# Kernel tuning notes

Measured on AMD Instinct MI355X. Metric: run time of the kernel, lower is better.

The kernel has to match this reference:

```python
import jax, jax.numpy as jnp
import numpy as np


def setup_inputs() -> dict:
    key = jax.random.key(0)
    k1, k2 = jax.random.split(key)
    B, T, F = 16, 4096, 512
    x = jax.random.normal(k1, (B, T, F), dtype=jnp.float32)
    probs = jax.random.uniform(k2, (B,), dtype=jnp.float32)  # per-row CDF value
    return {"x": x, "probs": probs}


def reference(x, probs):
    # SMALL_VALUE_MASKING + SUM_BASED scaling (training=True path).
    B = x.shape[0]
    n = x[0].size  # elements per batch row (time*feat)
    flat = x.reshape(B, -1)
    sorted_flat = jnp.sort(flat, axis=1)
    # index = max(ceil(n * prob) - 1, 0), per batch row
    idx = jnp.maximum(jnp.ceil(jnp.float32(n) * probs).astype(jnp.int32) - 1, 0)
    threshold = jnp.take_along_axis(sorted_flat, idx[:, None], axis=1)  # [B,1]
    threshold = threshold.reshape((B,) + (1,) * (x.ndim - 1))  # [B,1,1]
    # mask = 1 - (x < threshold): zero out values strictly below the quantile
    mask = 1.0 - (x < threshold).astype(x.dtype)
    out = x * mask
    # sum-based rescaling: |sum(x) / sum(out)| per row, divide_no_nan semantics
    reduce_axes = tuple(range(1, x.ndim))
    num = jnp.sum(x, axis=reduce_axes)
    den = jnp.sum(out, axis=reduce_axes)
    scale = jnp.abs(jnp.where(den == 0, jnp.zeros_like(num), num / den))
    scale = scale.reshape((B,) + (1,) * (x.ndim - 1))
    return scale * out
```

## Files before the change

### kernel.cpp

```cpp
#include <hip/hip_runtime.h>
#include <stdint.h>

#define THREADS 256
#define EPB     65536
#define NBINS   4096
#define ITERS   (EPB / 4 / THREADS)
#define CNT_STRIDE 16
#define LDSCAP  8192
#define K4T     1024

typedef float vfloat4 __attribute__((ext_vector_type(4)));

__device__ __forceinline__ uint32_t f2u(float f) {
    uint32_t b = __float_as_uint(f);
    return (b & 0x80000000u) ? ~b : (b | 0x80000000u);
}
__device__ __forceinline__ float u2f(uint32_t u) {
    uint32_t b = (u & 0x80000000u) ? (u & 0x7FFFFFFFu) : ~u;
    return __uint_as_float(b);
}

__device__ __forceinline__ double blockReduceSum(double v) {
    for (int off = 32; off > 0; off >>= 1) v += __shfl_down(v, off, 64);
    __shared__ double wsum[16];
    int lane = threadIdx.x & 63, wid = threadIdx.x >> 6;
    if (lane == 0) wsum[wid] = v;
    __syncthreads();
    double r = 0.0;
    if (threadIdx.x == 0) {
        int nw = (int)(blockDim.x >> 6);
        for (int i = 0; i < nw; ++i) r += wsum[i];
    }
    return r;
}

__global__ void __launch_bounds__(THREADS) k0_zero(uint4* __restrict__ p, int n16) {
    int idx = blockIdx.x * THREADS + threadIdx.x;
    int stride = gridDim.x * THREADS;
    uint4 z = {0u, 0u, 0u, 0u};
    for (int i = idx; i < n16; i += stride) p[i] = z;
}

__global__ void __launch_bounds__(THREADS) k1_hist(
    const float* __restrict__ x, uint32_t* __restrict__ ghist,
    double* __restrict__ rowSum, int blocksPerRow, int n) {
    __shared__ uint32_t hist[NBINS];
    for (int i = threadIdx.x; i < NBINS; i += THREADS) hist[i] = 0;
    __syncthreads();

    int row   = blockIdx.x / blocksPerRow;
    int chunk = blockIdx.x % blocksPerRow;
    const float4* p = (const float4*)(x + (size_t)row * n + (size_t)chunk * EPB);

    double s = 0.0;
    #pragma unroll 4
    for (int it = 0; it < ITERS; ++it) {
        float4 v = p[it * THREADS + threadIdx.x];
        s += (double)v.x + (double)v.y + (double)v.z + (double)v.w;
        atomicAdd(&hist[f2u(v.x) >> 20], 1u);
        atomicAdd(&hist[f2u(v.y) >> 20], 1u);
        atomicAdd(&hist[f2u(v.z) >> 20], 1u);
        atomicAdd(&hist[f2u(v.w) >> 20], 1u);
    }
    __syncthreads();

    uint32_t* gh = ghist + (size_t)row * NBINS;
    for (int i = threadIdx.x; i < NBINS; i += THREADS) {
        uint32_t c = hist[i];
        if (c) atomicAdd(&gh[i], c);
    }
    double bs = blockReduceSum(s);
    if (threadIdx.x == 0) atomicAdd(&rowSum[row], bs);
}

__global__ void __launch_bounds__(THREADS) k2_select(
    const uint32_t* __restrict__ ghist, const float* __restrict__ probs,
    uint32_t* __restrict__ aStar, uint32_t* __restrict__ rankW, int n) {
    int row = blockIdx.x;
    const uint32_t* h = ghist + (size_t)row * NBINS;
    __shared__ uint32_t part[THREADS];
    uint32_t s = 0;
    #pragma unroll
    for (int i = 0; i < NBINS / THREADS; ++i) s += h[threadIdx.x * (NBINS / THREADS) + i];
    part[threadIdx.x] = s;
    __syncthreads();
    if (threadIdx.x == 0) {
        float p = probs[row];
        float t = ceilf((float)n * p);
        long long idx = (long long)t - 1;
        if (idx < 0) idx = 0;
        uint32_t k = (uint32_t)idx + 1;
        uint32_t cum = 0;
        int chunk = 0;
        for (; chunk < THREADS - 1; ++chunk) {
            if (cum + part[chunk] >= k) break;
            cum += part[chunk];
        }
        int bin = chunk * (NBINS / THREADS);
        for (;; ++bin) {
            uint32_t c = h[bin];
            if (cum + c >= k || bin == NBINS - 1) break;
            cum += c;
        }
        aStar[row] = (uint32_t)bin;
        rankW[row] = k - cum;
    }
}

__global__ void __launch_bounds__(THREADS) k3_cand(
    const float* __restrict__ x, const uint32_t* __restrict__ aStar,
    uint32_t* __restrict__ cand, uint32_t* __restrict__ candCount,
    double* __restrict__ rowSumGt, int blocksPerRow, int cap, int n) {
    __shared__ uint32_t lbuf[LDSCAP];
    __shared__ uint32_t lcnt;
    __shared__ uint32_t gbase;
    if (threadIdx.x == 0) lcnt = 0;
    __syncthreads();

    int row   = blockIdx.x / blocksPerRow;
    int chunk = blockIdx.x % blocksPerRow;
    uint32_t a = aStar[row];
    uint32_t* cl = cand + (size_t)row * cap;
    uint32_t* cc = candCount + (size_t)row * CNT_STRIDE;
    const float4* p = (const float4*)(x + (size_t)row * n + (size_t)chunk * EPB);

    double s = 0.0;
    #pragma unroll 4
    for (int it = 0; it < ITERS; ++it) {
        float4 v = p[it * THREADS + threadIdx.x];
        float vals[4] = {v.x, v.y, v.z, v.w};
        #pragma unroll
        for (int j = 0; j < 4; ++j) {
            uint32_t u = f2u(vals[j]);
            uint32_t b = u >> 20;
            if (b > a) s += (double)vals[j];
            else if (b == a) {
                uint32_t pos = atomicAdd(&lcnt, 1u);
                if (pos < LDSCAP) lbuf[pos] = u;
                else {
                    uint32_t g = atomicAdd(cc, 1u);
                    if ((int)g < cap) cl[g] = u;
                }
            }
        }
    }
    __syncthreads();
    uint32_t cnt = (lcnt < LDSCAP) ? lcnt : LDSCAP;
    if (threadIdx.x == 0) gbase = atomicAdd(cc, cnt);
    __syncthreads();
    uint32_t base = gbase;
    for (uint32_t i = threadIdx.x; i < cnt; i += THREADS) {
        uint32_t g = base + i;
        if ((int)g < cap) cl[g] = lbuf[i];
    }
    double bs = blockReduceSum(s);
    if (threadIdx.x == 0) atomicAdd(&rowSumGt[row], bs);
}

__global__ void __launch_bounds__(K4T) k4_final(
    const uint32_t* __restrict__ cand, const uint32_t* __restrict__ candCount,
    const uint32_t* __restrict__ aStar, const uint32_t* __restrict__ rankW,
    const double* __restrict__ rowSum, const double* __restrict__ rowSumGt,
    float* __restrict__ scaleArr, float* __restrict__ thrArr, int cap) {
    int row = blockIdx.x, tid = threadIdx.x;
    uint32_t c = candCount[(size_t)row * CNT_STRIDE];
    if (c > (uint32_t)cap) c = (uint32_t)cap;
    const uint32_t* cl = cand + (size_t)row * cap;

    __shared__ uint32_t hcnt[4096];
    __shared__ double   hsum[4096];
    __shared__ uint32_t part1[K4T];
    __shared__ uint32_t part2[64];
    __shared__ uint32_t cnt256[256];
    __shared__ double   sum256[256];
    __shared__ uint32_t sh_b1, sh_r2, sh_b2;

    for (int i = tid; i < 4096; i += K4T) { hcnt[i] = 0; hsum[i] = 0.0; }
    for (int i = tid; i < 256;  i += K4T) { cnt256[i] = 0; sum256[i] = 0.0; }
    __syncthreads();

    for (uint32_t i = tid; i < c; i += K4T) {
        uint32_t u = cl[i];
        uint32_t b = (u >> 8) & 0xFFFu;
        atomicAdd(&hcnt[b], 1u);
        atomicAdd(&hsum[b], (double)u2f(u));
    }
    __syncthreads();

    uint32_t p1 = hcnt[tid*4] + hcnt[tid*4+1] + hcnt[tid*4+2] + hcnt[tid*4+3];
    part1[tid] = p1;
    __syncthreads();
    if (tid < 64) {
        uint32_t s2 = 0;
        for (int j = 0; j < 16; ++j) s2 += part1[tid*16 + j];
        part2[tid] = s2;
    }
    __syncthreads();
    if (tid == 0) {
        uint32_t r = rankW[row];
        uint32_t cum = 0;
        int j = 0;
        for (; j < 63; ++j) { if (cum + part2[j] >= r) break; cum += part2[j]; }
        int t = j * 16;
        for (; t < j*16 + 15; ++t) { if (cum + part1[t] >= r) break; cum += part1[t]; }
        int b = t * 4;
        for (; b < t*4 + 3; ++b) { if (cum + hcnt[b] >= r) break; cum += hcnt[b]; }
        sh_b1 = (uint32_t)b;
        sh_r2 = r - cum;
    }
    __syncthreads();
    uint32_t b1 = sh_b1;

    double g = 0.0;
    for (int i = tid; i < 4096; i += K4T) if (i > (int)b1) g += hsum[i];

    for (uint32_t i = tid; i < c; i += K4T) {
        uint32_t u = cl[i];
        if (((u >> 8) & 0xFFFu) == b1) {
            atomicAdd(&cnt256[u & 0xFFu], 1u);
            atomicAdd(&sum256[u & 0xFFu], (double)u2f(u));
        }
    }
    __syncthreads();
    if (tid == 0) {
        uint32_t r2 = sh_r2, cum = 0;
        int b = 0;
        for (; b < 255; ++b) { if (cum + cnt256[b] >= r2) break; cum += cnt256[b]; }
        sh_b2 = (uint32_t)b;
    }
    __syncthreads();
    uint32_t b2 = sh_b2;
    uint32_t uthr = (aStar[row] << 20) | (b1 << 8) | b2;

    double g2 = 0.0;
    for (int i = tid; i < 256; i += K4T) if (i > (int)b2) g2 += sum256[i];

    double tot = blockReduceSum(g + g2);
    if (tid == 0) {
        tot += (double)cnt256[b2] * (double)u2f(uthr);
        double den = rowSumGt[row] + tot;
        double num = rowSum[row];
        double sc  = (den == 0.0) ? 0.0 : fabs(num / den);
        scaleArr[row] = (float)sc;
        thrArr[row]   = u2f(uthr);
    }
}

__global__ void __launch_bounds__(THREADS) k5_out(
    const float* __restrict__ x, float* __restrict__ out,
    const float* __restrict__ scaleArr, const float* __restrict__ thrArr,
    int blocksPerRow, int n) {
    int row   = blockIdx.x / blocksPerRow;
    int chunk = blockIdx.x % blocksPerRow;
    float sc = scaleArr[row];
    float th = thrArr[row];
    size_t base = (size_t)row * n + (size_t)chunk * EPB;
    const float4* p = (const float4*)(x + base);
    vfloat4* o = (vfloat4*)(out + base);
    #pragma unroll 4
    for (int it = 0; it < ITERS; ++it) {
        float4 v = p[it * THREADS + threadIdx.x];
        vfloat4 w;
        w.x = (v.x < th) ? 0.0f : v.x * sc;
        w.y = (v.y < th) ? 0.0f : v.y * sc;
        w.z = (v.z < th) ? 0.0f : v.z * sc;
        w.w = (v.w < th) ? 0.0f : v.w * sc;
        __builtin_nontemporal_store(w, &o[it * THREADS + threadIdx.x]);
    }
}

extern "C" void kernel_launch(void* const* d_in, const int* in_sizes, int n_in,
                              void* d_out, int out_size, void* d_ws, size_t ws_size,
                              hipStream_t stream) {
    const float* x     = (const float*)d_in[0];
    const float* probs = (const float*)d_in[1];
    float* out = (float*)d_out;

    int B = in_sizes[1];
    long long total = in_sizes[0];
    int n = (int)(total / B);
    int blocksPerRow = n / EPB;

    uint8_t* ws = (uint8_t*)d_ws;
    size_t off = 0;
    uint32_t* ghist = (uint32_t*)(ws + off); off += (size_t)B * NBINS * 4;
    double* rowSum    = (double*)(ws + off); off += (size_t)B * 8;
    double* rowSumGt  = (double*)(ws + off); off += (size_t)B * 8;
    uint32_t* aStar   = (uint32_t*)(ws + off); off += (size_t)B * 4;
    uint32_t* rankW   = (uint32_t*)(ws + off); off += (size_t)B * 4;
    uint32_t* candCnt = (uint32_t*)(ws + off); off += (size_t)B * CNT_STRIDE * 4;
    float* scaleArr   = (float*)(ws + off); off += (size_t)B * 4;
    float* thrArr     = (float*)(ws + off); off += (size_t)B * 4;
    off = (off + 255) & ~(size_t)255;
    size_t zeroBytes = off;
    size_t remain = (ws_size > off) ? (ws_size - off) : 0;
    int cap = (int)(remain / ((size_t)B * 4));
    if (cap > 262144) cap = 262144;
    if (cap < 1) cap = 1;
    uint32_t* cand = (uint32_t*)(ws + off);

    int n16 = (int)(zeroBytes / 16);
    k0_zero  <<<128,              THREADS, 0, stream>>>((uint4*)d_ws, n16);

    k1_hist  <<<B * blocksPerRow, THREADS, 0, stream>>>(x, ghist, rowSum, blocksPerRow, n);
    k2_select<<<B,                THREADS, 0, stream>>>(ghist, probs, aStar, rankW, n);
    k3_cand  <<<B * blocksPerRow, THREADS, 0, stream>>>(x, aStar, cand, candCnt, rowSumGt,
                                                        blocksPerRow, cap, n);
    k4_final <<<B,                K4T,     0, stream>>>(cand, candCnt, aStar, rankW,
                                                        rowSum, rowSumGt, scaleArr, thrArr, cap);
    k5_out   <<<B * blocksPerRow, THREADS, 0, stream>>>(x, out, scaleArr, thrArr, blocksPerRow, n);
}
```

Baseline: 188.5 us.

## Predict quantile bin window by sampling and fuse histogram with candidate pass

Adds a sampling kernel that builds a coarse histogram from every 64th float4 of each row and picks a window of top-12-bit bins that should contain the target quantile. The histogram pass and the candidate-collection pass are fused into one kernel that reads x once, collecting all values inside the window, so the second full read of x is skipped. If the true bin falls outside the window or candidates overflow, a fallback kernel redoes the old exact candidate pass. The final kernel filters candidates back to the true bin and adds the sum of above-bin window values. The cost is a larger candidate buffer, extra LDS and atomics in the main pass, and the launch overhead of the sampling and fallback kernels.

```diff
diff --git a/kernel.cpp b/kernel.cpp
--- a/kernel.cpp
+++ b/kernel.cpp
@@ -8,6 +8,8 @@
 #define CNT_STRIDE 16
 #define LDSCAP  8192
 #define K4T     1024
+#define SAMPLE_STRIDE 64
+#define SMARGIN 600
 
 typedef float vfloat4 __attribute__((ext_vector_type(4)));
 
@@ -41,41 +43,127 @@
     for (int i = idx; i < n16; i += stride) p[i] = z;
 }
 
-__global__ void __launch_bounds__(THREADS) k1_hist(
-    const float* __restrict__ x, uint32_t* __restrict__ ghist,
-    double* __restrict__ rowSum, int blocksPerRow, int n) {
+__global__ void __launch_bounds__(THREADS) kS_window(
+    const float* __restrict__ x, const float* __restrict__ probs,
+    uint32_t* __restrict__ winLo, uint32_t* __restrict__ winHi, int n) {
+    int row = blockIdx.x;
     __shared__ uint32_t hist[NBINS];
+    __shared__ uint32_t part[THREADS];
     for (int i = threadIdx.x; i < NBINS; i += THREADS) hist[i] = 0;
     __syncthreads();
-
-    int row   = blockIdx.x / blocksPerRow;
-    int chunk = blockIdx.x % blocksPerRow;
-    const float4* p = (const float4*)(x + (size_t)row * n + (size_t)chunk * EPB);
-
-    double s = 0.0;
-    #pragma unroll 4
-    for (int it = 0; it < ITERS; ++it) {
-        float4 v = p[it * THREADS + threadIdx.x];
-        s += (double)v.x + (double)v.y + (double)v.z + (double)v.w;
+    const float4* p = (const float4*)(x + (size_t)row * n);
+    int nf4 = n / 4;
+    int ns4 = nf4 / SAMPLE_STRIDE;
+    for (int i = threadIdx.x; i < ns4; i += THREADS) {
+        float4 v = p[(size_t)i * SAMPLE_STRIDE];
         atomicAdd(&hist[f2u(v.x) >> 20], 1u);
         atomicAdd(&hist[f2u(v.y) >> 20], 1u);
         atomicAdd(&hist[f2u(v.z) >> 20], 1u);
         atomicAdd(&hist[f2u(v.w) >> 20], 1u);
     }
     __syncthreads();
-
+    uint32_t sLoc = 0;
+    for (int j = 0; j < NBINS / THREADS; ++j) sLoc += hist[threadIdx.x * (NBINS / THREADS) + j];
+    part[threadIdx.x] = sLoc;
+    __syncthreads();
+    if (threadIdx.x == 0) {
+        long long nS = (long long)ns4 * 4;
+        float pr = probs[row];
+        float t = ceilf((float)n * pr);
+        long long idx = (long long)t - 1; if (idx < 0) idx = 0;
+        unsigned long long k = (unsigned long long)idx + 1;
+        long long rS = (long long)((k * (unsigned long long)nS) / (unsigned long long)n);
+        long long loT = rS - SMARGIN;
+        long long hiT = rS + SMARGIN;
+        int lo, hi;
+        if (loT <= 0) lo = 0;
+        else {
+            uint32_t T = (uint32_t)loT, cum = 0; int ch = 0;
+            for (; ch < THREADS - 1; ++ch) { if (cum + part[ch] >= T) break; cum += part[ch]; }
+            int b = ch * (NBINS / THREADS);
+            for (;; ++b) { uint32_t cb = hist[b]; if (cum + cb >= T || b == NBINS - 1) break; cum += cb; }
+            lo = b;
+        }
+        if (hiT >= nS) hi = NBINS - 1;
+        else {
+            uint32_t T = (uint32_t)hiT, cum = 0; int ch = 0;
+            for (; ch < THREADS - 1; ++ch) { if (cum + part[ch] >= T) break; cum += part[ch]; }
+            int b = ch * (NBINS / THREADS);
+            for (;; ++b) { uint32_t cb = hist[b]; if (cum + cb >= T || b == NBINS - 1) break; cum += cb; }
+            hi = b;
+        }
+        if (hi < lo) hi = lo;
+        winLo[row] = (uint32_t)lo;
+        winHi[row] = (uint32_t)hi;
+    }
+}
+
+__global__ void __launch_bounds__(THREADS) k13_main(
+    const float* __restrict__ x, const uint32_t* __restrict__ winLo,
+    const uint32_t* __restrict__ winHi, uint32_t* __restrict__ ghist,
+    double* __restrict__ rowSum, double* __restrict__ rowSumGtWin,
+    uint32_t* __restrict__ cand, uint32_t* __restrict__ candCount,
+    int blocksPerRow, int cap, int n) {
+    __shared__ uint32_t hist[NBINS];
+    __shared__ uint32_t lbuf[LDSCAP];
+    __shared__ uint32_t lcnt, gbase;
+    for (int i = threadIdx.x; i < NBINS; i += THREADS) hist[i] = 0;
+    if (threadIdx.x == 0) lcnt = 0;
+    __syncthreads();
+
+    int row   = blockIdx.x / blocksPerRow;
+    int chunk = blockIdx.x % blocksPerRow;
+    uint32_t lo = winLo[row], hi = winHi[row];
+    uint32_t* cl = cand + (size_t)row * cap;
+    uint32_t* cc = candCount + (size_t)row * CNT_STRIDE;
+    const float4* p = (const float4*)(x + (size_t)row * n + (size_t)chunk * EPB);
+
+    double s = 0.0, sGt = 0.0;
+    #pragma unroll 4
+    for (int it = 0; it < ITERS; ++it) {
+        float4 v = p[it * THREADS + threadIdx.x];
+        float vals[4] = {v.x, v.y, v.z, v.w};
+        #pragma unroll
+        for (int j = 0; j < 4; ++j) {
+            uint32_t u = f2u(vals[j]);
+            uint32_t b = u >> 20;
+            atomicAdd(&hist[b], 1u);
+            s += (double)vals[j];
+            if (b > hi) sGt += (double)vals[j];
+            else if (b >= lo) {
+                uint32_t pos = atomicAdd(&lcnt, 1u);
+                if (pos < LDSCAP) lbuf[pos] = u;
+                else { uint32_t g = atomicAdd(cc, 1u); if ((int)g < cap) cl[g] = u; }
+            }
+        }
+    }
+    __syncthreads();
     uint32_t* gh = ghist + (size_t)row * NBINS;
     for (int i = threadIdx.x; i < NBINS; i += THREADS) {
-        uint32_t c = hist[i];
-        if (c) atomicAdd(&gh[i], c);
+        uint32_t hv = hist[i];
+        if (hv) atomicAdd(&gh[i], hv);
+    }
+    uint32_t cnt = (lcnt < LDSCAP) ? lcnt : LDSCAP;
+    if (threadIdx.x == 0) gbase = atomicAdd(cc, cnt);
+    __syncthreads();
+    uint32_t base = gbase;
+    for (uint32_t i = threadIdx.x; i < cnt; i += THREADS) {
+        uint32_t g = base + i;
+        if ((int)g < cap) cl[g] = lbuf[i];
     }
     double bs = blockReduceSum(s);
     if (threadIdx.x == 0) atomicAdd(&rowSum[row], bs);
+    __syncthreads();
+    double bg = blockReduceSum(sGt);
+    if (threadIdx.x == 0) atomicAdd(&rowSumGtWin[row], bg);
 }
 
 __global__ void __launch_bounds__(THREADS) k2_select(
     const uint32_t* __restrict__ ghist, const float* __restrict__ probs,
-    uint32_t* __restrict__ aStar, uint32_t* __restrict__ rankW, int n) {
+    uint32_t* __restrict__ aStar, uint32_t* __restrict__ rankW,
+    uint32_t* __restrict__ candCnt, const uint32_t* __restrict__ winLo,
+    const uint32_t* __restrict__ winHi, uint32_t* __restrict__ flagOk,
+    int cap, int n) {
     int row = blockIdx.x;
     const uint32_t* h = ghist + (size_t)row * NBINS;
     __shared__ uint32_t part[THREADS];
@@ -104,27 +192,32 @@
         }
         aStar[row] = (uint32_t)bin;
         rankW[row] = k - cum;
-    }
-}
-
-__global__ void __launch_bounds__(THREADS) k3_cand(
+        uint32_t ccv = candCnt[(size_t)row * CNT_STRIDE];
+        int ok = (bin >= (int)winLo[row] && bin <= (int)winHi[row] &&
+                  ccv <= (uint32_t)cap) ? 1 : 0;
+        flagOk[row] = (uint32_t)ok;
+        if (!ok) candCnt[(size_t)row * CNT_STRIDE] = 0;
+    }
+}
+
+__global__ void __launch_bounds__(THREADS) k3_fallback(
     const float* __restrict__ x, const uint32_t* __restrict__ aStar,
+    const uint32_t* __restrict__ flagOk,
     uint32_t* __restrict__ cand, uint32_t* __restrict__ candCount,
-    double* __restrict__ rowSumGt, int blocksPerRow, int cap, int n) {
+    double* __restrict__ rowSumGtFB, int blocksPerRow, int cap, int n) {
+    int row   = blockIdx.x / blocksPerRow;
+    if (flagOk[row]) return;
     __shared__ uint32_t lbuf[LDSCAP];
-    __shared__ uint32_t lcnt;
-    __shared__ uint32_t gbase;
+    __shared__ uint32_t lcnt, gbase;
     if (threadIdx.x == 0) lcnt = 0;
     __syncthreads();
-
-    int row   = blockIdx.x / blocksPerRow;
     int chunk = blockIdx.x % blocksPerRow;
     uint32_t a = aStar[row];
     uint32_t* cl = cand + (size_t)row * cap;
     uint32_t* cc = candCount + (size_t)row * CNT_STRIDE;
     const float4* p = (const float4*)(x + (size_t)row * n + (size_t)chunk * EPB);
 
-    double s = 0.0;
+    double sg = 0.0;
     #pragma unroll 4
     for (int it = 0; it < ITERS; ++it) {
         float4 v = p[it * THREADS + threadIdx.x];
@@ -133,14 +226,11 @@
         for (int j = 0; j < 4; ++j) {
             uint32_t u = f2u(vals[j]);
             uint32_t b = u >> 20;
-            if (b > a) s += (double)vals[j];
+            if (b > a) sg += (double)vals[j];
             else if (b == a) {
                 uint32_t pos = atomicAdd(&lcnt, 1u);
                 if (pos < LDSCAP) lbuf[pos] = u;
-                else {
-                    uint32_t g = atomicAdd(cc, 1u);
-                    if ((int)g < cap) cl[g] = u;
-                }
+                else { uint32_t g = atomicAdd(cc, 1u); if ((int)g < cap) cl[g] = u; }
             }
         }
     }
@@ -153,19 +243,21 @@
         uint32_t g = base + i;
         if ((int)g < cap) cl[g] = lbuf[i];
     }
-    double bs = blockReduceSum(s);
-    if (threadIdx.x == 0) atomicAdd(&rowSumGt[row], bs);
+    double bs = blockReduceSum(sg);
+    if (threadIdx.x == 0) atomicAdd(&rowSumGtFB[row], bs);
 }
 
 __global__ void __launch_bounds__(K4T) k4_final(
     const uint32_t* __restrict__ cand, const uint32_t* __restrict__ candCount,
     const uint32_t* __restrict__ aStar, const uint32_t* __restrict__ rankW,
-    const double* __restrict__ rowSum, const double* __restrict__ rowSumGt,
+    const double* __restrict__ rowSum, const double* __restrict__ rowSumGtWin,
+    const double* __restrict__ rowSumGtFB, const uint32_t* __restrict__ flagOk,
     float* __restrict__ scaleArr, float* __restrict__ thrArr, int cap) {
     int row = blockIdx.x, tid = threadIdx.x;
     uint32_t c = candCount[(size_t)row * CNT_STRIDE];
     if (c > (uint32_t)cap) c = (uint32_t)cap;
     const uint32_t* cl = cand + (size_t)row * cap;
+    uint32_t a = aStar[row];
 
     __shared__ uint32_t hcnt[4096];
     __shared__ double   hsum[4096];
@@ -179,11 +271,17 @@
     for (int i = tid; i < 256;  i += K4T) { cnt256[i] = 0; sum256[i] = 0.0; }
     __syncthreads();
 
+    double sMid = 0.0;
     for (uint32_t i = tid; i < c; i += K4T) {
         uint32_t u = cl[i];
-        uint32_t b = (u >> 8) & 0xFFFu;
-        atomicAdd(&hcnt[b], 1u);
-        atomicAdd(&hsum[b], (double)u2f(u));
+        uint32_t cb = u >> 20;
+        if (cb == a) {
+            uint32_t b = (u >> 8) & 0xFFFu;
+            atomicAdd(&hcnt[b], 1u);
+            atomicAdd(&hsum[b], (double)u2f(u));
+        } else if (cb > a) {
+            sMid += (double)u2f(u);
+        }
     }
     __syncthreads();
 
@@ -197,8 +295,7 @@
     }
     __syncthreads();
     if (tid == 0) {
-        uint32_t r = rankW[row];
-        uint32_t cum = 0;
+        uint32_t r = rankW[row], cum = 0;
         int j = 0;
         for (; j < 63; ++j) { if (cum + part2[j] >= r) break; cum += part2[j]; }
         int t = j * 16;
@@ -216,7 +313,7 @@
 
     for (uint32_t i = tid; i < c; i += K4T) {
         uint32_t u = cl[i];
-        if (((u >> 8) & 0xFFFu) == b1) {
+        if ((u >> 20) == a && ((u >> 8) & 0xFFFu) == b1) {
             atomicAdd(&cnt256[u & 0xFFu], 1u);
             atomicAdd(&sum256[u & 0xFFu], (double)u2f(u));
         }
@@ -230,15 +327,16 @@
     }
     __syncthreads();
     uint32_t b2 = sh_b2;
-    uint32_t uthr = (aStar[row] << 20) | (b1 << 8) | b2;
+    uint32_t uthr = (a << 20) | (b1 << 8) | b2;
 
     double g2 = 0.0;
     for (int i = tid; i < 256; i += K4T) if (i > (int)b2) g2 += sum256[i];
 
-    double tot = blockReduceSum(g + g2);
+    double tot = blockReduceSum(g + g2 + sMid);
     if (tid == 0) {
         tot += (double)cnt256[b2] * (double)u2f(uthr);
-        double den = rowSumGt[row] + tot;
+        double gtBase = flagOk[row] ? rowSumGtWin[row] : rowSumGtFB[row];
+        double den = gtBase + tot;
         double num = rowSum[row];
         double sc  = (den == 0.0) ? 0.0 : fabs(num / den);
         scaleArr[row] = (float)sc;
@@ -283,30 +381,39 @@
 
     uint8_t* ws = (uint8_t*)d_ws;
     size_t off = 0;
-    uint32_t* ghist = (uint32_t*)(ws + off); off += (size_t)B * NBINS * 4;
-    double* rowSum    = (double*)(ws + off); off += (size_t)B * 8;
-    double* rowSumGt  = (double*)(ws + off); off += (size_t)B * 8;
-    uint32_t* aStar   = (uint32_t*)(ws + off); off += (size_t)B * 4;
-    uint32_t* rankW   = (uint32_t*)(ws + off); off += (size_t)B * 4;
-    uint32_t* candCnt = (uint32_t*)(ws + off); off += (size_t)B * CNT_STRIDE * 4;
-    float* scaleArr   = (float*)(ws + off); off += (size_t)B * 4;
-    float* thrArr     = (float*)(ws + off); off += (size_t)B * 4;
+    uint32_t* ghist    = (uint32_t*)(ws + off); off += (size_t)B * NBINS * 4;
+    double* rowSum     = (double*)(ws + off);   off += (size_t)B * 8;
+    double* rowSumGtW  = (double*)(ws + off);   off += (size_t)B * 8;
+    double* rowSumGtFB = (double*)(ws + off);   off += (size_t)B * 8;
+    uint32_t* aStar    = (uint32_t*)(ws + off); off += (size_t)B * 4;
+    uint32_t* rankW    = (uint32_t*)(ws + off); off += (size_t)B * 4;
+    uint32_t* winLo    = (uint32_t*)(ws + off); off += (size_t)B * 4;
+    uint32_t* winHi    = (uint32_t*)(ws + off); off += (size_t)B * 4;
+    uint32_t* flagOk   = (uint32_t*)(ws + off); off += (size_t)B * 4;
+    uint32_t* candCnt  = (uint32_t*)(ws + off); off += (size_t)B * CNT_STRIDE * 4;
+    float* scaleArr    = (float*)(ws + off);    off += (size_t)B * 4;
+    float* thrArr      = (float*)(ws + off);    off += (size_t)B * 4;
     off = (off + 255) & ~(size_t)255;
     size_t zeroBytes = off;
     size_t remain = (ws_size > off) ? (ws_size - off) : 0;
     int cap = (int)(remain / ((size_t)B * 4));
-    if (cap > 262144) cap = 262144;
+    if (cap > (1 << 20)) cap = (1 << 20);
     if (cap < 1) cap = 1;
     uint32_t* cand = (uint32_t*)(ws + off);
 
     int n16 = (int)(zeroBytes / 16);
-    k0_zero  <<<128,              THREADS, 0, stream>>>((uint4*)d_ws, n16);
-
-    k1_hist  <<<B * blocksPerRow, THREADS, 0, stream>>>(x, ghist, rowSum, blocksPerRow, n);
-    k2_select<<<B,                THREADS, 0, stream>>>(ghist, probs, aStar, rankW, n);
-    k3_cand  <<<B * blocksPerRow, THREADS, 0, stream>>>(x, aStar, cand, candCnt, rowSumGt,
-                                                        blocksPerRow, cap, n);
-    k4_final <<<B,                K4T,     0, stream>>>(cand, candCnt, aStar, rankW,
-                                                        rowSum, rowSumGt, scaleArr, thrArr, cap);
-    k5_out   <<<B * blocksPerRow, THREADS, 0, stream>>>(x, out, scaleArr, thrArr, blocksPerRow, n);
-}
+    k0_zero    <<<128,              THREADS, 0, stream>>>((uint4*)d_ws, n16);
+    kS_window  <<<B,                THREADS, 0, stream>>>(x, probs, winLo, winHi, n);
+    k13_main   <<<B * blocksPerRow, THREADS, 0, stream>>>(x, winLo, winHi, ghist, rowSum,
+                                                          rowSumGtW, cand, candCnt,
+                                                          blocksPerRow, cap, n);
+    k2_select  <<<B,                THREADS, 0, stream>>>(ghist, probs, aStar, rankW,
+                                                          candCnt, winLo, winHi, flagOk, cap, n);
+    k3_fallback<<<B * blocksPerRow, THREADS, 0, stream>>>(x, aStar, flagOk, cand, candCnt,
+                                                          rowSumGtFB, blocksPerRow, cap, n);
+    k4_final   <<<B,                K4T,     0, stream>>>(cand, candCnt, aStar, rankW,
+                                                          rowSum, rowSumGtW, rowSumGtFB, flagOk,
+                                                          scaleArr, thrArr, cap);
+    k5_out     <<<B * blocksPerRow, THREADS, 0, stream>>>(x, out, scaleArr, thrArr,
+                                                          blocksPerRow, n);
+}
```

Measured after the change: 258.3 us. 1.37x slower.
